# Performance work log

Measured on AMD Instinct MI355X. Metric: run time of the kernel, lower is better.

The kernel has to match this reference:

```python
import jax, jax.numpy as jnp
import numpy as np

N_EMBED = 2048
N_HEAD = 16
N_KV_HEAD = 4
HEAD_DIM = N_EMBED // N_HEAD
REPEAT = N_HEAD // N_KV_HEAD
THETA = 10000.0


def setup_inputs() -> dict:
    key = jax.random.key(0)
    ks = jax.random.split(key, 9)
    B, T = 2, 2048
    s = 0.02
    return {
        'x': jax.random.normal(ks[0], (B, T, N_EMBED), jnp.float32),
        'Wq': jax.random.normal(ks[1], (N_EMBED, N_EMBED), jnp.float32) * s,
        'bq': jax.random.normal(ks[2], (N_EMBED,), jnp.float32) * s,
        'Wk': jax.random.normal(ks[3], (N_EMBED, N_KV_HEAD * HEAD_DIM), jnp.float32) * s,
        'bk': jax.random.normal(ks[4], (N_KV_HEAD * HEAD_DIM,), jnp.float32) * s,
        'Wv': jax.random.normal(ks[5], (N_EMBED, N_KV_HEAD * HEAD_DIM), jnp.float32) * s,
        'bv': jax.random.normal(ks[6], (N_KV_HEAD * HEAD_DIM,), jnp.float32) * s,
        'Wo': jax.random.normal(ks[7], (N_EMBED, N_EMBED), jnp.float32) * s,
        'bo': jax.random.normal(ks[8], (N_EMBED,), jnp.float32) * s,
    }


def _rope_angles(T):
    # Quirk of original: freqs exponent uses full n_embed, then sliced to head_dim//2
    freqs = THETA ** (-(jnp.arange(0, N_EMBED, 2, dtype=jnp.float32) / N_EMBED))
    freqs = freqs[: HEAD_DIM // 2]
    t = jnp.arange(T, dtype=jnp.float32)
    return jnp.outer(t, freqs)  # [T, HEAD_DIM//2]


def _apply_rope(x, cos, sin):
    # x: [B, T, H, D]; pairs are adjacent elements along D
    xr = x[..., 0::2]
    xi = x[..., 1::2]
    # cos/sin: [1, T, 1, D//2]
    or_ = xr * cos - xi * sin
    oi_ = xr * sin + xi * cos
    out = jnp.stack([or_, oi_], axis=-1).reshape(x.shape)
    # original casts rope output to bfloat16
    return out.astype(jnp.bfloat16).astype(jnp.float32)


def reference(x, Wq, bq, Wk, bk, Wv, bv, Wo, bo):
    B, T, _ = x.shape
    q = (x @ Wq + bq).reshape(B, T, N_HEAD, HEAD_DIM)
    k = (x @ Wk + bk).reshape(B, T, N_KV_HEAD, HEAD_DIM)
    v = (x @ Wv + bv).reshape(B, T, N_KV_HEAD, HEAD_DIM)

    ang = _rope_angles(T)
    cos = jnp.cos(ang)[None, :, None, :]
    sin = jnp.sin(ang)[None, :, None, :]
    xq = _apply_rope(q, cos, sin)
    xk = _apply_rope(k, cos, sin)

    xq = xq.transpose(0, 2, 1, 3)                 # [B, H, T, D]
    xk = xk.transpose(0, 2, 1, 3)                 # [B, Hkv, T, D]
    xv = v.transpose(0, 2, 1, 3)                  # [B, Hkv, T, D]
    xk = jnp.repeat(xk, REPEAT, axis=1)           # [B, H, T, D]
    xv = jnp.repeat(xv, REPEAT, axis=1)

    qk = jnp.einsum('bhtd,bhsd->bhts', xq, xk)    # [B, H, T, T]
    causal = jnp.tril(jnp.ones((T, T), dtype=bool))
    qk = jnp.where(causal[None, None], qk, -jnp.inf)
    # Quirk: scale applied AFTER softmax, using n_embed**-0.5
    attn = jax.nn.softmax(qk, axis=-1) * (N_EMBED ** -0.5)
    o = jnp.einsum('bhts,bhsd->bhtd', attn, xv)
    o = o.transpose(0, 2, 1, 3).reshape(B, T, N_EMBED)
    return o @ Wo + bo
```

## Files before the change

### kernel.cpp

```cpp
#include <hip/hip_runtime.h>
#include <stdint.h>
#include <math.h>

typedef unsigned short u16;
typedef __attribute__((ext_vector_type(8))) short short8;
typedef __attribute__((ext_vector_type(8))) _Float16 half8;
typedef __attribute__((ext_vector_type(4))) float float4v;
typedef __attribute__((ext_vector_type(16))) float float16v;
typedef __attribute__((ext_vector_type(4))) u16 ushort4v;

#define T_SEQ 2048
#define NB 2
#define NE 2048
#define NH 16
#define NKV 4
#define HD 128
#define KDIM 2048

union Frag { short8 s; half8 h; };

__device__ inline u16 f32_bf16(float f) {
    union { float f; uint32_t u; } v; v.f = f;
    uint32_t u = v.u;
    return (u16)((u + 0x7fffu + ((u >> 16) & 1u)) >> 16);
}
__device__ inline u16 f32_f16(float f) {
    union { _Float16 h; u16 u; } v; v.h = (_Float16)f;
    return v.u;
}

__device__ inline uint32_t cvtpk_bf16(float lo, float hi) {
    uint32_t r;
    asm("v_cvt_pk_bf16_f32 %0, %1, %2" : "=v"(r) : "v"(lo), "v"(hi));
    return r;
}
__device__ inline void perm32swap(uint32_t& a, uint32_t& b) {
    asm("v_permlane32_swap_b32 %0, %1" : "+v"(a), "+v"(b));
}

typedef __attribute__((address_space(1))) const void g_void;
typedef __attribute__((address_space(3))) void l_void;
#define GLOAD16(g, l) __builtin_amdgcn_global_load_lds((g_void*)(g), (l_void*)(l), 16, 0, 0)

__global__ void conv_f16(const float* __restrict__ in, u16* __restrict__ out) {
    int i = blockIdx.x * blockDim.x + threadIdx.x;
    float4 v = ((const float4*)in)[i];
    ushort4v o;
    o.x = f32_f16(v.x); o.y = f32_f16(v.y); o.z = f32_f16(v.z); o.w = f32_f16(v.w);
    *(ushort4v*)(out + (size_t)i * 4) = o;
}

template<bool TO_F16>
__global__ void transpose_convert(const float* __restrict__ in, u16* __restrict__ out,
                                  int K, int N) {
    __shared__ float tile[32][33];
    int n0 = blockIdx.x * 32, k0 = blockIdx.y * 32;
    int tx = threadIdx.x, ty = threadIdx.y;
    for (int i = 0; i < 32; i += 8)
        tile[ty + i][tx] = in[(size_t)(k0 + ty + i) * N + n0 + tx];
    __syncthreads();
    for (int i = 0; i < 32; i += 8) {
        float v = tile[tx][ty + i];
        out[(size_t)(n0 + ty + i) * K + k0 + tx] = TO_F16 ? f32_f16(v) : f32_bf16(v);
    }
}

__global__ void rope_tab(float* __restrict__ ctab, float* __restrict__ stab) {
    int i = blockIdx.x * blockDim.x + threadIdx.x;
    int t = i >> 6, j = i & 63;
    float freqf = (float)pow(10000.0, -(double)j / 1024.0);
    float angf = (float)t * freqf;
    double a = (double)angf;
    ctab[i] = (float)cos(a);
    stab[i] = (float)sin(a);
}

#define GEMM_STAGE_DECL(Asrc, Bsrc) \
    int rin = lane >> 2, ksl = lane & 3; \
    int u0r = wid * 32; \
    const u16* Ag0 = (Asrc) + (size_t)(m0 + u0r + rin) * KDIM + ksl * 8; \
    const u16* Ag1 = (Asrc) + (size_t)(m0 + u0r + 16 + rin) * KDIM + ksl * 8; \
    const u16* Bg0 = (Bsrc) + (size_t)(n0 + u0r + rin) * KDIM + ksl * 8; \
    const u16* Bg1 = (Bsrc) + (size_t)(n0 + u0r + 16 + rin) * KDIM + ksl * 8;

#define GEMM_STAGE(Abuf, Bbuf, kk) \
    GLOAD16(Ag0 + (kk), &Abuf[u0r * 32]); \
    GLOAD16(Ag1 + (kk), &Abuf[(u0r + 16) * 32]); \
    GLOAD16(Bg0 + (kk), &Bbuf[u0r * 32]); \
    GLOAD16(Bg1 + (kk), &Bbuf[(u0r + 16) * 32]);

#define GEMM_COMPUTE(Abuf, Bbuf, F16) { \
    Frag af[4], bf[4]; \
    for (int i = 0; i < 4; i++) \
        af[i].s = *(const short8*)&Abuf[(wr * 64 + i * 16 + l16) * 32 + quad * 8]; \
    for (int j = 0; j < 4; j++) \
        bf[j].s = *(const short8*)&Bbuf[(wc * 64 + j * 16 + l16) * 32 + quad * 8]; \
    for (int i = 0; i < 4; i++) \
        for (int j = 0; j < 4; j++) { \
            if (F16) \
                acc[i][j] = __builtin_amdgcn_mfma_f32_16x16x32_f16(af[i].h, bf[j].h, acc[i][j], 0, 0, 0); \
            else \
                acc[i][j] = __builtin_amdgcn_mfma_f32_16x16x32_bf16(af[i].s, bf[j].s, acc[i][j], 0, 0, 0); \
        } \
}

#define GEMM_MAINLOOP(F16) \
    GEMM_STAGE(Alds0, Blds0, 0) \
    __syncthreads(); \
    for (int k0 = 0; k0 < KDIM; k0 += 64) { \
        GEMM_STAGE(Alds1, Blds1, k0 + 32) \
        GEMM_COMPUTE(Alds0, Blds0, F16) \
        __syncthreads(); \
        if (k0 + 64 < KDIM) { GEMM_STAGE(Alds0, Blds0, k0 + 64) } \
        GEMM_COMPUTE(Alds1, Blds1, F16) \
        __syncthreads(); \
    }

__global__ __launch_bounds__(256)
void gemm_qkv(const u16* __restrict__ xh, const u16* __restrict__ wqt,
              const u16* __restrict__ wkt, const u16* __restrict__ wvt,
              const float* __restrict__ bq, const float* __restrict__ bk,
              const float* __restrict__ bv,
              u16* __restrict__ qout, u16* __restrict__ kout, u16* __restrict__ vout,
              const float* __restrict__ ctab, const float* __restrict__ stab) {
    __shared__ u16 Alds0[128 * 32], Alds1[128 * 32];
    __shared__ u16 Blds0[128 * 32], Blds1[128 * 32];
    int tid = threadIdx.x;
    int wid = tid >> 6, lane = tid & 63;
    int quad = lane >> 4, l16 = lane & 15;
    int wr = wid >> 1, wc = wid & 1;

    int lin = blockIdx.x;
    int mode, m0, n0;
    const u16 *A, *Bt;
    if (lin < 512) {
        mode = 0; m0 = (lin >> 4) * 128; n0 = (lin & 15) * 128; A = xh; Bt = wqt;
    } else if (lin < 640) {
        int i = lin - 512;
        mode = 1; m0 = (i >> 2) * 128; n0 = (i & 3) * 128; A = xh; Bt = wkt;
    } else {
        int i = lin - 640;
        mode = 2; m0 = (i & 3) * 128; n0 = (i >> 2) * 128; A = wvt; Bt = xh;
    }

    float4v acc[4][4];
    for (int i = 0; i < 4; i++) for (int j = 0; j < 4; j++) acc[i][j] = (float4v){0,0,0,0};

    GEMM_STAGE_DECL(A, Bt)
    GEMM_MAINLOOP(true)

    if (mode == 2) {
        for (int i = 0; i < 4; i++) {
            int mbase = m0 + wr * 64 + i * 16 + quad * 4;
            float brow[4];
            for (int r = 0; r < 4; r++) brow[r] = bv[mbase + r];
            for (int j = 0; j < 4; j++) {
                int col = n0 + wc * 64 + j * 16 + l16;
                int b = col >> 11, t = col & 2047;
                for (int r = 0; r < 4; r++) {
                    int m = mbase + r;
                    float val = acc[i][j][r] + brow[r];
                    vout[(((size_t)(b * NKV + (m >> 7))) * HD + (m & 127)) * T_SEQ + t] = f32_bf16(val);
                }
            }
        }
    } else {
        const float* bias = mode ? bk : bq;
        u16* outU = mode ? kout : qout;
        int nheads = mode ? NKV : NH;
        for (int i = 0; i < 4; i++) {
            int mbase = m0 + wr * 64 + i * 16 + quad * 4;
            for (int j = 0; j < 4; j++) {
                int col = n0 + wc * 64 + j * 16 + l16;
                float bcol = bias[col];
                for (int r = 0; r < 4; r++) {
                    int m = mbase + r;
                    float val = acc[i][j][r] + bcol;
                    int b = m >> 11, t = m & 2047;
                    int h = col >> 7, d = col & 127;
                    int jj = d >> 1;
                    float c = ctab[t * 64 + jj];
                    float s = stab[t * 64 + jj];
                    float partner = __shfl_xor(val, 1, 64);
                    float o = (d & 1) ? (partner * s + val * c) : (val * c - partner * s);
                    outU[(((size_t)(b * nheads + h)) * T_SEQ + t) * HD + d] = f32_bf16(o);
                }
            }
        }
    }
}

__global__ __launch_bounds__(256)
void gemm_out(const u16* __restrict__ A, const u16* __restrict__ Bt,
              const float* __restrict__ bias, float* __restrict__ outF) {
    __shared__ u16 Alds0[128 * 32], Alds1[128 * 32];
    __shared__ u16 Blds0[128 * 32], Blds1[128 * 32];
    int tid = threadIdx.x;
    int wid = tid >> 6, lane = tid & 63;
    int quad = lane >> 4, l16 = lane & 15;
    int wr = wid >> 1, wc = wid & 1;
    int m0 = blockIdx.x * 128, n0 = blockIdx.y * 128;

    float4v acc[4][4];
    for (int i = 0; i < 4; i++) for (int j = 0; j < 4; j++) acc[i][j] = (float4v){0,0,0,0};

    GEMM_STAGE_DECL(A, Bt)
    GEMM_MAINLOOP(false)

    for (int i = 0; i < 4; i++) {
        int mbase = m0 + wr * 64 + i * 16 + quad * 4;
        for (int j = 0; j < 4; j++) {
            int col = n0 + wc * 64 + j * 16 + l16;
            float bcol = bias[col];
            for (int r = 0; r < 4; r++)
                outF[(size_t)(mbase + r) * NE + col] = acc[i][j][r] + bcol;
        }
    }
}

__global__ __launch_bounds__(256, 2)
void attn_kernel(const u16* __restrict__ Qr, const u16* __restrict__ Kr,
                 const u16* __restrict__ Vt, u16* __restrict__ Oout) {
    __shared__ u16 smem[17920];
    u16* klds = smem;
    u16* vlds = smem + 8704;
    int tid = threadIdx.x;
    int wid = tid >> 6, lane = tid & 63;
    int l32 = lane & 31, hh = lane >> 5;

    int lin = blockIdx.x + (blockIdx.y << 4);
    int g = lin >> 5, bh = lin & 31;
    int qt = (lin < 256) ? (15 - g) : (g - 8);
    int b = bh >> 4, hd = bh & 15, kvh = hd >> 2;
    int t0 = qt * 128;

    const u16* Qb = Qr + (((size_t)(b * NH + hd)) * T_SEQ + t0 + wid * 32) * HD;
    const u16* Kb = Kr + ((size_t)(b * NKV + kvh)) * T_SEQ * HD;
    const u16* Vb = Vt + ((size_t)(b * NKV + kvh)) * HD * T_SEQ;

    short8 qf[8];
#pragma unroll
    for (int ks = 0; ks < 8; ks++)
        qf[ks] = *(const short8*)(Qb + (size_t)l32 * HD + ks * 16 + hh * 8);

    float16v oacc[4];
#pragma unroll
    for (int dt = 0; dt < 4; dt++)
        oacc[dt] = (float16v){0,0,0,0,0,0,0,0,0,0,0,0,0,0,0,0};
    float m_run = -INFINITY, l_run = 0.f;

    int ksr = tid >> 2, kc = (tid & 3) * 32;
    int vdr = tid >> 1, vc = (tid & 1) * 32;

    int nst = 2 * qt + 2;

    {
        const u16* ksrc = Kb + (size_t)ksr * HD + kc;
        const u16* vsrc = Vb + (size_t)vdr * T_SEQ + vc;
        short8 kr0[4], vr0[4];
#pragma unroll
        for (int i = 0; i < 4; i++) kr0[i] = *(const short8*)(ksrc + i * 8);
#pragma unroll
        for (int i = 0; i < 4; i++) vr0[i] = *(const short8*)(vsrc + i * 8);
#pragma unroll
        for (int i = 0; i < 4; i++) *(short8*)&klds[ksr * 136 + kc + i * 8] = kr0[i];
#pragma unroll
        for (int i = 0; i < 4; i++) *(short8*)&vlds[vdr * 72 + vc + i * 8] = vr0[i];
    }
    __syncthreads();

    for (int st = 0; st < nst; st++) {
        short8 krg[4], vrg[4];
        bool more = (st + 1 < nst);
        if (more) {
            const u16* ksrc = Kb + ((size_t)(st + 1) * 64 + ksr) * HD + kc;
            const u16* vsrc = Vb + (size_t)vdr * T_SEQ + (st + 1) * 64 + vc;
#pragma unroll
            for (int i = 0; i < 4; i++) krg[i] = *(const short8*)(ksrc + i * 8);
#pragma unroll
            for (int i = 0; i < 4; i++) vrg[i] = *(const short8*)(vsrc + i * 8);
        }

        bool active = (st * 64) <= (t0 + wid * 32 + 31);
        if (active) {
            float16v sfa[2];
            sfa[0] = (float16v){0,0,0,0,0,0,0,0,0,0,0,0,0,0,0,0};
            sfa[1] = (float16v){0,0,0,0,0,0,0,0,0,0,0,0,0,0,0,0};
            __builtin_amdgcn_s_setprio(1);
#pragma unroll
            for (int ks = 0; ks < 8; ks++) {
                short8 kf0 = *(const short8*)&klds[l32 * 136 + ks * 16 + hh * 8];
                short8 kf1 = *(const short8*)&klds[(32 + l32) * 136 + ks * 16 + hh * 8];
                sfa[0] = __builtin_amdgcn_mfma_f32_32x32x16_bf16(kf0, qf[ks], sfa[0], 0, 0, 0);
                sfa[1] = __builtin_amdgcn_mfma_f32_32x32x16_bf16(kf1, qf[ks], sfa[1], 0, 0, 0);
            }
            __builtin_amdgcn_s_setprio(0);

            int tg = t0 + wid * 32 + l32;
            if (st >= 2 * qt) {
#pragma unroll
                for (int stile = 0; stile < 2; stile++)
#pragma unroll
                    for (int r = 0; r < 16; r++) {
                        int s = st * 64 + stile * 32 + (r & 3) + 8 * (r >> 2) + 4 * hh;
                        if (s > tg) sfa[stile][r] = -INFINITY;
                    }
            }

            float mx = -INFINITY;
#pragma unroll
            for (int stile = 0; stile < 2; stile++)
#pragma unroll
                for (int r = 0; r < 16; r++) mx = fmaxf(mx, sfa[stile][r]);
            mx = fmaxf(mx, __shfl_xor(mx, 32, 64));
            bool nos = __all(mx - m_run <= 8.f);
            float mnew = nos ? m_run : fmaxf(m_run, mx);
            float alpha = nos ? 1.f : __expf(m_run - mnew);
            float psum = 0.f;
#pragma unroll
            for (int stile = 0; stile < 2; stile++)
#pragma unroll
                for (int r = 0; r < 16; r++) {
                    float p = __expf(sfa[stile][r] - mnew);
                    sfa[stile][r] = p;
                    psum += p;
                }
            psum += __shfl_xor(psum, 32, 64);
            l_run = l_run * alpha + psum;
            m_run = mnew;

            if (!nos) {
#pragma unroll
                for (int dt = 0; dt < 4; dt++)
#pragma unroll
                    for (int r = 0; r < 16; r++) oacc[dt][r] *= alpha;
            }

            __builtin_amdgcn_s_setprio(1);
#pragma unroll
            for (int g2 = 0; g2 < 4; g2++) {
                int stile = g2 >> 1, gg = g2 & 1;
                uint32_t P0 = cvtpk_bf16(sfa[stile][8 * gg + 0], sfa[stile][8 * gg + 1]);
                uint32_t P1 = cvtpk_bf16(sfa[stile][8 * gg + 2], sfa[stile][8 * gg + 3]);
                uint32_t P2 = cvtpk_bf16(sfa[stile][8 * gg + 4], sfa[stile][8 * gg + 5]);
                uint32_t P3 = cvtpk_bf16(sfa[stile][8 * gg + 6], sfa[stile][8 * gg + 7]);
                perm32swap(P0, P2);
                perm32swap(P1, P3);
                union { uint32_t w[4]; short8 s; } pf;
                pf.w[0] = P0; pf.w[1] = P1; pf.w[2] = P2; pf.w[3] = P3;
#pragma unroll
                for (int dt = 0; dt < 4; dt++) {
                    short8 vf = *(const short8*)&vlds[(dt * 32 + l32) * 72 + g2 * 16 + hh * 8];
                    oacc[dt] = __builtin_amdgcn_mfma_f32_32x32x16_bf16(vf, pf.s, oacc[dt], 0, 0, 0);
                }
            }
            __builtin_amdgcn_s_setprio(0);
        }

        __syncthreads();
        if (more) {
#pragma unroll
            for (int i = 0; i < 4; i++) *(short8*)&klds[ksr * 136 + kc + i * 8] = krg[i];
#pragma unroll
            for (int i = 0; i < 4; i++) *(short8*)&vlds[vdr * 72 + vc + i * 8] = vrg[i];
        }
        __syncthreads();
    }

    const float scale = 0.022097086912079608f;
    float sc = scale / l_run;
    u16* ow = smem + wid * 4352;
#pragma unroll
    for (int dt = 0; dt < 4; dt++)
#pragma unroll
        for (int gq = 0; gq < 4; gq++) {
            ushort4v pk;
            pk.x = f32_bf16(oacc[dt][gq * 4 + 0] * sc);
            pk.y = f32_bf16(oacc[dt][gq * 4 + 1] * sc);
            pk.z = f32_bf16(oacc[dt][gq * 4 + 2] * sc);
            pk.w = f32_bf16(oacc[dt][gq * 4 + 3] * sc);
            *(ushort4v*)&ow[l32 * 136 + dt * 32 + gq * 8 + hh * 4] = pk;
        }
    __syncthreads();
    int tl = lane >> 4, dcol = (lane & 15) * 8;
#pragma unroll
    for (int ch = 0; ch < 8; ch++) {
        int t_local = tl + ch * 4;
        short8 ov = *(const short8*)&ow[t_local * 136 + dcol];
        *(short8*)&Oout[((size_t)(b * T_SEQ) + t0 + wid * 32 + t_local) * NE + hd * HD + dcol] = ov;
    }
}

extern "C" void kernel_launch(void* const* d_in, const int* in_sizes, int n_in,
                              void* d_out, int out_size, void* d_ws, size_t ws_size,
                              hipStream_t stream) {
    const float* x  = (const float*)d_in[0];
    const float* Wq = (const float*)d_in[1];
    const float* bq = (const float*)d_in[2];
    const float* Wk = (const float*)d_in[3];
    const float* bk = (const float*)d_in[4];
    const float* Wv = (const float*)d_in[5];
    const float* bv = (const float*)d_in[6];
    const float* Wo = (const float*)d_in[7];
    const float* bo = (const float*)d_in[8];
    float* out = (float*)d_out;
    char* ws = (char*)d_ws;

    u16* xh   = (u16*)(ws);
    u16* wqt  = (u16*)(ws + 16777216);
    u16* wkt  = (u16*)(ws + 25165824);
    u16* wvt  = (u16*)(ws + 27262976);
    u16* qr   = (u16*)(ws + 29360128);
    u16* kr   = (u16*)(ws + 46137344);
    u16* vt   = (u16*)(ws + 50331648);
    float* ctab = (float*)(ws + 54525952);
    float* stab = (float*)(ws + 55050240);
    u16* ao  = xh;
    u16* wot = wqt;

    conv_f16<<<8192, 256, 0, stream>>>(x, xh);
    transpose_convert<true><<<dim3(64, 64), dim3(32, 8), 0, stream>>>(Wq, wqt, 2048, 2048);
    transpose_convert<true><<<dim3(16, 64), dim3(32, 8), 0, stream>>>(Wk, wkt, 2048, 512);
    transpose_convert<true><<<dim3(16, 64), dim3(32, 8), 0, stream>>>(Wv, wvt, 2048, 512);
    rope_tab<<<512, 256, 0, stream>>>(ctab, stab);

    gemm_qkv<<<dim3(768), 256, 0, stream>>>(xh, wqt, wkt, wvt, bq, bk, bv,
                                            qr, kr, vt, ctab, stab);

    transpose_convert<false><<<dim3(64, 64), dim3(32, 8), 0, stream>>>(Wo, wot, 2048, 2048);

    attn_kernel<<<dim3(16, 32), 256, 0, stream>>>(qr, kr, vt, ao);

    gemm_out<<<dim3(32, 16), 256, 0, stream>>>(ao, wot, bo, out);
}
```

Before: 330.3 us.

## Use partial vmcnt waits in GEMM pipeline and XCD-aware block remapping

```diff
diff --git a/kernel.cpp b/kernel.cpp
--- a/kernel.cpp
+++ b/kernel.cpp
@@ -74,6 +74,22 @@
     ctab[i] = (float)cos(a);
     stab[i] = (float)sin(a);
 }
+
+#define GEMM_WAITBAR4() \
+    __builtin_amdgcn_sched_barrier(0); \
+    asm volatile("s_waitcnt vmcnt(4)" ::: "memory"); \
+    asm volatile("s_barrier" ::: "memory"); \
+    __builtin_amdgcn_sched_barrier(0);
+#define GEMM_WAITBAR0() \
+    __builtin_amdgcn_sched_barrier(0); \
+    asm volatile("s_waitcnt vmcnt(0)" ::: "memory"); \
+    asm volatile("s_barrier" ::: "memory"); \
+    __builtin_amdgcn_sched_barrier(0);
+#define GEMM_READBAR() \
+    __builtin_amdgcn_sched_barrier(0); \
+    asm volatile("s_waitcnt lgkmcnt(0)" ::: "memory"); \
+    asm volatile("s_barrier" ::: "memory"); \
+    __builtin_amdgcn_sched_barrier(0);
 
 #define GEMM_STAGE_DECL(Asrc, Bsrc) \
     int rin = lane >> 2, ksl = lane & 3; \
@@ -106,14 +122,19 @@
 
 #define GEMM_MAINLOOP(F16) \
     GEMM_STAGE(Alds0, Blds0, 0) \
-    __syncthreads(); \
     for (int k0 = 0; k0 < KDIM; k0 += 64) { \
         GEMM_STAGE(Alds1, Blds1, k0 + 32) \
+        GEMM_WAITBAR4()                  \
         GEMM_COMPUTE(Alds0, Blds0, F16) \
-        __syncthreads(); \
-        if (k0 + 64 < KDIM) { GEMM_STAGE(Alds0, Blds0, k0 + 64) } \
+        GEMM_READBAR()                   \
+        if (k0 + 64 < KDIM) { \
+            GEMM_STAGE(Alds0, Blds0, k0 + 64) \
+            GEMM_WAITBAR4()              \
+        } else { \
+            GEMM_WAITBAR0()              \
+        } \
         GEMM_COMPUTE(Alds1, Blds1, F16) \
-        __syncthreads(); \
+        GEMM_READBAR() \
     }
 
 __global__ __launch_bounds__(256)
@@ -130,7 +151,8 @@
     int quad = lane >> 4, l16 = lane & 15;
     int wr = wid >> 1, wc = wid & 1;
 
-    int lin = blockIdx.x;
+    int bid = blockIdx.x;
+    int lin = (bid & 7) * 96 + (bid >> 3);
     int mode, m0, n0;
     const u16 *A, *Bt;
     if (lin < 512) {
@@ -199,7 +221,9 @@
     int wid = tid >> 6, lane = tid & 63;
     int quad = lane >> 4, l16 = lane & 15;
     int wr = wid >> 1, wc = wid & 1;
-    int m0 = blockIdx.x * 128, n0 = blockIdx.y * 128;
+    int bid = blockIdx.x;
+    int lin = (bid & 7) * 64 + (bid >> 3);
+    int m0 = (lin >> 4) * 128, n0 = (lin & 15) * 128;
 
     float4v acc[4][4];
     for (int i = 0; i < 4; i++) for (int j = 0; j < 4; j++) acc[i][j] = (float4v){0,0,0,0};
@@ -431,5 +455,5 @@
 
     attn_kernel<<<dim3(16, 32), 256, 0, stream>>>(qr, kr, vt, ao);
 
-    gemm_out<<<dim3(32, 16), 256, 0, stream>>>(ao, wot, bo, out);
-}
+    gemm_out<<<dim3(512), 256, 0, stream>>>(ao, wot, bo, out);
+}
```

After: 332.8 us. Within noise of the previous version (+0.8%).
